# Performance work log

Measured on AMD Instinct MI355X. Metric: run time of the kernel, lower is better.

The kernel has to match this reference:

```python
import jax, jax.numpy as jnp
import numpy as np

N_NODES = 100000
N_EDGES = 1600000
D = 64
LN_EPS = 1e-5


def gcn_layer(x, src, dst, adv, W, b, g, be):
    # message: softmax(log(adv), dst) == adv / segment_sum(adv)[dst]  (per-target-node normalization)
    denom = jax.ops.segment_sum(adv, dst, num_segments=N_NODES)  # [N]
    att = adv / denom[dst]                                       # [E]
    msg = x[src] * att[:, None]                                  # [E, D] gather-multiply
    aggr = jax.ops.segment_sum(msg, dst, num_segments=N_NODES)   # [N, D] scatter-add
    # update: LayerNorm(Dropout(Linear(gelu(aggr) + x)))  (dropout = identity in eval)
    h = jax.nn.gelu(aggr, approximate=False) + x
    h = h @ W + b
    mu = jnp.mean(h, axis=-1, keepdims=True)
    var = jnp.mean((h - mu) ** 2, axis=-1, keepdims=True)
    return (h - mu) * jax.lax.rsqrt(var + LN_EPS) * g + be


def setup_inputs() -> dict:
    key = jax.random.key(0)
    ks = jax.random.split(key, 8)
    scale = 1.0 / np.sqrt(D)
    node_attr = jax.random.normal(ks[0], (N_NODES, D), jnp.float32)
    edge_index = jax.random.randint(ks[1], (2, N_EDGES), 0, N_NODES)
    batch_idx = jnp.zeros((N_NODES,), jnp.int32)
    adv_att0 = jax.random.uniform(ks[2], (N_EDGES,), jnp.float32) + 1e-3
    adv_att1 = jax.random.uniform(ks[3], (N_EDGES,), jnp.float32) + 1e-3
    W0 = jax.random.uniform(ks[4], (D, D), jnp.float32, -scale, scale)
    W1 = jax.random.uniform(ks[5], (D, D), jnp.float32, -scale, scale)
    b0 = jnp.zeros((D,), jnp.float32)
    b1 = jnp.zeros((D,), jnp.float32)
    g0 = jnp.ones((D,), jnp.float32)
    g1 = jnp.ones((D,), jnp.float32)
    be0 = jnp.zeros((D,), jnp.float32)
    be1 = jnp.zeros((D,), jnp.float32)
    return {"node_attr": node_attr, "edge_index": edge_index, "batch_idx": batch_idx,
            "adv_att0": adv_att0, "adv_att1": adv_att1,
            "W0": W0, "b0": b0, "g0": g0, "be0": be0,
            "W1": W1, "b1": b1, "g1": g1, "be1": be1}


def reference(node_attr, edge_index, batch_idx, adv_att0, adv_att1,
              W0, b0, g0, be0, W1, b1, g1, be1):
    src = edge_index[0]  # j (source)
    dst = edge_index[1]  # i (target)
    h = gcn_layer(node_attr, src, dst, adv_att0, W0, b0, g0, be0)
    h = gcn_layer(h, src, dst, adv_att1, W1, b1, g1, be1)
    return h  # node_level=True -> per-node representations [N, D]
```

## Files before the change

kernel.cpp:

```cpp
#include <hip/hip_runtime.h>
#include <math.h>

#define N_NODES 100000
#define N_EDGES 1600000
#define D 64
#define LN_EPS 1e-5f
#define NQ (N_EDGES / 4)
#define NODE_RANGE 12500
#define CAP 48

typedef int v2i __attribute__((ext_vector_type(2)));
typedef int v4i __attribute__((ext_vector_type(4)));

__device__ __forceinline__ unsigned short f2b(float f) {
    unsigned u = __float_as_uint(f);
    return (unsigned short)((u + 0x7FFFu + ((u >> 16) & 1u)) >> 16);
}
__device__ __forceinline__ unsigned pk2(float lo, float hi) {
    return (unsigned)f2b(lo) | ((unsigned)f2b(hi) << 16);
}
__device__ __forceinline__ float b2f(unsigned short u) {
    return __uint_as_float((unsigned)u << 16);
}

__global__ void k_tobf16z(const float4* __restrict__ in4, uint4* __restrict__ out4,
                          int* __restrict__ cnt) {
    int i = blockIdx.x * 256 + threadIdx.x;
    if (i < N_NODES) cnt[i] = 0;
    float4 a = in4[2 * i];
    float4 c = in4[2 * i + 1];
    uint4 o;
    o.x = pk2(a.x, a.y);
    o.y = pk2(a.z, a.w);
    o.z = pk2(c.x, c.y);
    o.w = pk2(c.z, c.w);
    out4[i] = o;
}

__global__ void k_bucket(const int* __restrict__ src, const v4i* __restrict__ dst4,
                         const float* __restrict__ adv0, const float* __restrict__ adv1,
                         int* __restrict__ cnt, v2i* __restrict__ rec) {
    const int g = blockIdx.x & 7;
    const int lb = blockIdx.x >> 3;
    const int nlb = gridDim.x >> 3;
    const int lo = g * NODE_RANGE, hi = lo + NODE_RANGE;
    for (int q = lb * 256 + threadIdx.x; q < NQ; q += nlb * 256) {
        v4i d = dst4[q];
        int e = q * 4;
#pragma unroll
        for (int c = 0; c < 4; ++c) {
            int dd = (c == 0) ? d.x : (c == 1) ? d.y : (c == 2) ? d.z : d.w;
            if (dd >= lo && dd < hi) {
                int p = atomicAdd(&cnt[dd], 1);
                if (p < CAP) {
                    int s = src[e + c];
                    float a0 = adv0[e + c];
                    float a1 = adv1[e + c];
                    v2i r;
                    r.x = s;
                    r.y = (int)pk2(a0, a1);
                    __builtin_nontemporal_store(r, &rec[(size_t)p * N_NODES + dd]);
                }
            }
        }
    }
}

template <int LAYER>
__global__ __launch_bounds__(256) void k_layer(const float* __restrict__ xres,
                                               const unsigned short* __restrict__ xb,
                                               const v2i* __restrict__ rec,
                                               const int* __restrict__ cnt,
                                               const float* __restrict__ W,
                                               const float* __restrict__ bb,
                                               const float* __restrict__ gg,
                                               const float* __restrict__ be,
                                               float* __restrict__ outf,
                                               unsigned short* __restrict__ outb) {
    const int lane = threadIdx.x & 63;
    const int wid = threadIdx.x >> 6;
    const int nodeA = blockIdx.x * 8 + wid;
    const int nodeB = nodeA + 4;
    const int nA = min(cnt[nodeA], CAP);
    const int nB = min(cnt[nodeB], CAP);

    const int slot = lane >> 3;
    const int fgrp = lane & 7;
    const int bpbase = slot << 2;

    float accA[8], accB[8];
#pragma unroll
    for (int i = 0; i < 8; ++i) { accA[i] = 0.f; accB[i] = 0.f; }

    int svA = 0, aviA = 0, svB = 0, aviB = 0;
    if (lane < nA) {
        v2i r = rec[(size_t)lane * N_NODES + nodeA];
        svA = r.x;
        unsigned pa = (unsigned)r.y;
        aviA = (int)(LAYER ? (pa & 0xFFFF0000u) : (pa << 16));
    }
    if (lane < nB) {
        v2i r = rec[(size_t)lane * N_NODES + nodeB];
        svB = r.x;
        unsigned pa = (unsigned)r.y;
        aviB = (int)(LAYER ? (pa & 0xFFFF0000u) : (pa << 16));
    }
    float sadvA = __int_as_float(aviA);
    float sadvB = __int_as_float(aviB);

    const int nmax = max(nA, nB);
    for (int j0 = 0; j0 < nmax; j0 += 8) {
        const int idx = (j0 << 2) + bpbase;
        if (j0 < nA) {
            int s = __builtin_amdgcn_ds_bpermute(idx, svA);
            float a = __int_as_float(__builtin_amdgcn_ds_bpermute(idx, aviA));
            uint4 u = *(const uint4*)(xb + (unsigned)s * D + (fgrp << 3));
            accA[0] = fmaf(__uint_as_float(u.x << 16), a, accA[0]);
            accA[1] = fmaf(__uint_as_float(u.x & 0xFFFF0000u), a, accA[1]);
            accA[2] = fmaf(__uint_as_float(u.y << 16), a, accA[2]);
            accA[3] = fmaf(__uint_as_float(u.y & 0xFFFF0000u), a, accA[3]);
            accA[4] = fmaf(__uint_as_float(u.z << 16), a, accA[4]);
            accA[5] = fmaf(__uint_as_float(u.z & 0xFFFF0000u), a, accA[5]);
            accA[6] = fmaf(__uint_as_float(u.w << 16), a, accA[6]);
            accA[7] = fmaf(__uint_as_float(u.w & 0xFFFF0000u), a, accA[7]);
        }
        if (j0 < nB) {
            int s = __builtin_amdgcn_ds_bpermute(idx, svB);
            float a = __int_as_float(__builtin_amdgcn_ds_bpermute(idx, aviB));
            uint4 u = *(const uint4*)(xb + (unsigned)s * D + (fgrp << 3));
            accB[0] = fmaf(__uint_as_float(u.x << 16), a, accB[0]);
            accB[1] = fmaf(__uint_as_float(u.x & 0xFFFF0000u), a, accB[1]);
            accB[2] = fmaf(__uint_as_float(u.y << 16), a, accB[2]);
            accB[3] = fmaf(__uint_as_float(u.y & 0xFFFF0000u), a, accB[3]);
            accB[4] = fmaf(__uint_as_float(u.z << 16), a, accB[4]);
            accB[5] = fmaf(__uint_as_float(u.z & 0xFFFF0000u), a, accB[5]);
            accB[6] = fmaf(__uint_as_float(u.w << 16), a, accB[6]);
            accB[7] = fmaf(__uint_as_float(u.w & 0xFFFF0000u), a, accB[7]);
        }
    }
#pragma unroll
    for (int m = 8; m <= 32; m <<= 1) {
#pragma unroll
        for (int i = 0; i < 8; ++i) {
            accA[i] += __shfl_xor(accA[i], m, 64);
            accB[i] += __shfl_xor(accB[i], m, 64);
        }
    }
    for (int m = 32; m; m >>= 1) {
        sadvA += __shfl_xor(sadvA, m, 64);
        sadvB += __shfl_xor(sadvB, m, 64);
    }

    __shared__ float hs[8][D];
    __shared__ float pp[4][8][D];
    if (slot == 0) {
#pragma unroll
        for (int i = 0; i < 8; ++i) {
            hs[wid][lane * 8 + i] = accA[i];
            hs[4 + wid][lane * 8 + i] = accB[i];
        }
    }
    float aggrA = (nA > 0) ? hs[wid][lane] / sadvA : 0.f;
    float aggrB = (nB > 0) ? hs[4 + wid][lane] / sadvB : 0.f;

    float xvA = (LAYER == 0) ? xres[(unsigned)(nodeA * D) + lane]
                             : b2f(xb[(unsigned)(nodeA * D) + lane]);
    float xvB = (LAYER == 0) ? xres[(unsigned)(nodeB * D) + lane]
                             : b2f(xb[(unsigned)(nodeB * D) + lane]);
    float geA = 0.5f * aggrA;
    float geB = 0.5f * aggrB;
    hs[wid][lane] = fmaf(geA, erff(aggrA * 0.70710678118654752f), geA + xvA);
    hs[4 + wid][lane] = fmaf(geB, erff(aggrB * 0.70710678118654752f), geB + xvB);
    __syncthreads();

    float py[8];
#pragma unroll
    for (int i = 0; i < 8; ++i) py[i] = 0.f;
    const float* wp = W + (wid * 16) * D + lane;
#pragma unroll
    for (int k4 = 0; k4 < 4; ++k4) {
        float w0 = wp[(k4 * 4 + 0) * D];
        float w1 = wp[(k4 * 4 + 1) * D];
        float w2 = wp[(k4 * 4 + 2) * D];
        float w3 = wp[(k4 * 4 + 3) * D];
#pragma unroll
        for (int nn = 0; nn < 8; ++nn) {
            float4 hv = *(const float4*)&hs[nn][wid * 16 + k4 * 4];
            py[nn] = fmaf(hv.x, w0, fmaf(hv.y, w1, fmaf(hv.z, w2, fmaf(hv.w, w3, py[nn]))));
        }
    }
#pragma unroll
    for (int nn = 0; nn < 8; ++nn) pp[wid][nn][lane] = py[nn];
    __syncthreads();

    const float bl = bb[lane], gl = gg[lane], bel = be[lane];
#pragma unroll
    for (int half = 0; half < 2; ++half) {
        const int row = wid + half * 4;
        const int node = blockIdx.x * 8 + row;
        float acc2 = bl + ((pp[0][row][lane] + pp[1][row][lane]) +
                           (pp[2][row][lane] + pp[3][row][lane]));
        float s = acc2;
        for (int m = 32; m; m >>= 1) s += __shfl_xor(s, m, 64);
        float mu = s * (1.f / 64.f);
        float dv = acc2 - mu;
        float v2 = dv * dv;
        for (int m = 32; m; m >>= 1) v2 += __shfl_xor(v2, m, 64);
        float var = v2 * (1.f / 64.f);
        float res = dv * rsqrtf(var + LN_EPS) * gl + bel;
        if (LAYER == 0)
            outb[(unsigned)(node * D) + lane] = f2b(res);
        else
            __builtin_nontemporal_store(res, outf + (unsigned)(node * D) + lane);
    }
}

extern "C" void kernel_launch(void* const* d_in, const int* in_sizes, int n_in,
                              void* d_out, int out_size, void* d_ws, size_t ws_size,
                              hipStream_t stream) {
    const float* node_attr = (const float*)d_in[0];
    const int* edge_index = (const int*)d_in[1];
    const float* adv0 = (const float*)d_in[3];
    const float* adv1 = (const float*)d_in[4];
    const float* W0 = (const float*)d_in[5];
    const float* b0 = (const float*)d_in[6];
    const float* g0 = (const float*)d_in[7];
    const float* be0 = (const float*)d_in[8];
    const float* W1 = (const float*)d_in[9];
    const float* b1 = (const float*)d_in[10];
    const float* g1 = (const float*)d_in[11];
    const float* be1 = (const float*)d_in[12];

    const int* src = edge_index;
    const v4i* dst4 = (const v4i*)(edge_index + N_EDGES);

    v2i* rec = (v2i*)d_ws;
    unsigned short* h1b = (unsigned short*)(rec + (size_t)N_NODES * CAP);
    int* cnt = (int*)(h1b + (size_t)N_NODES * D);

    float* out = (float*)d_out;
    unsigned short* xb0 = (unsigned short*)d_out;

    k_tobf16z<<<3125, 256, 0, stream>>>((const float4*)node_attr, (uint4*)xb0, cnt);

    k_bucket<<<4096, 256, 0, stream>>>(src, dst4, adv0, adv1, cnt, rec);

    k_layer<0><<<N_NODES / 8, 256, 0, stream>>>(node_attr, xb0, rec, cnt,
                                                W0, b0, g0, be0, nullptr, h1b);
    k_layer<1><<<N_NODES / 8, 256, 0, stream>>>(nullptr, h1b, rec, cnt,
                                                W1, b1, g1, be1, out, nullptr);
}
```

Measured before the change: 235.7 us.

## Make layer kernel persistent with register-resident weights and packed FMAs

Each layer kernel now runs a fixed grid of 2048 blocks that loop grid-stride over 8-node groups, instead of one block per group. Each thread loads its 16-row slice of W and the bias and LayerNorm parameters into registers once per block rather than once per group. The gather-accumulate loop now uses two-wide float vector FMAs, which may map to packed FP32 instructions. The aim is to cut block launch overhead and repeated weight loads. In exchange, register pressure rises and there may be fewer waves in flight to hide gather latency.

```diff
diff --git a/kernel.cpp b/kernel.cpp
--- a/kernel.cpp
+++ b/kernel.cpp
@@ -8,9 +8,11 @@
 #define NQ (N_EDGES / 4)
 #define NODE_RANGE 12500
 #define CAP 48
+#define NGRP (N_NODES / 8)
 
 typedef int v2i __attribute__((ext_vector_type(2)));
 typedef int v4i __attribute__((ext_vector_type(4)));
+typedef float v2f __attribute__((ext_vector_type(2)));
 
 __device__ __forceinline__ unsigned short f2b(float f) {
     unsigned u = __float_as_uint(f);
@@ -79,139 +81,154 @@
                                                unsigned short* __restrict__ outb) {
     const int lane = threadIdx.x & 63;
     const int wid = threadIdx.x >> 6;
-    const int nodeA = blockIdx.x * 8 + wid;
-    const int nodeB = nodeA + 4;
-    const int nA = min(cnt[nodeA], CAP);
-    const int nB = min(cnt[nodeB], CAP);
-
     const int slot = lane >> 3;
     const int fgrp = lane & 7;
     const int bpbase = slot << 2;
 
-    float accA[8], accB[8];
-#pragma unroll
-    for (int i = 0; i < 8; ++i) { accA[i] = 0.f; accB[i] = 0.f; }
-
-    int svA = 0, aviA = 0, svB = 0, aviB = 0;
-    if (lane < nA) {
-        v2i r = rec[(size_t)lane * N_NODES + nodeA];
-        svA = r.x;
-        unsigned pa = (unsigned)r.y;
-        aviA = (int)(LAYER ? (pa & 0xFFFF0000u) : (pa << 16));
+    float wreg[16];
+    {
+        const float* wp = W + (wid * 16) * D + lane;
+#pragma unroll
+        for (int k = 0; k < 16; ++k) wreg[k] = wp[k * D];
     }
-    if (lane < nB) {
-        v2i r = rec[(size_t)lane * N_NODES + nodeB];
-        svB = r.x;
-        unsigned pa = (unsigned)r.y;
-        aviB = (int)(LAYER ? (pa & 0xFFFF0000u) : (pa << 16));
-    }
-    float sadvA = __int_as_float(aviA);
-    float sadvB = __int_as_float(aviB);
-
-    const int nmax = max(nA, nB);
-    for (int j0 = 0; j0 < nmax; j0 += 8) {
-        const int idx = (j0 << 2) + bpbase;
-        if (j0 < nA) {
-            int s = __builtin_amdgcn_ds_bpermute(idx, svA);
-            float a = __int_as_float(__builtin_amdgcn_ds_bpermute(idx, aviA));
-            uint4 u = *(const uint4*)(xb + (unsigned)s * D + (fgrp << 3));
-            accA[0] = fmaf(__uint_as_float(u.x << 16), a, accA[0]);
-            accA[1] = fmaf(__uint_as_float(u.x & 0xFFFF0000u), a, accA[1]);
-            accA[2] = fmaf(__uint_as_float(u.y << 16), a, accA[2]);
-            accA[3] = fmaf(__uint_as_float(u.y & 0xFFFF0000u), a, accA[3]);
-            accA[4] = fmaf(__uint_as_float(u.z << 16), a, accA[4]);
-            accA[5] = fmaf(__uint_as_float(u.z & 0xFFFF0000u), a, accA[5]);
-            accA[6] = fmaf(__uint_as_float(u.w << 16), a, accA[6]);
-            accA[7] = fmaf(__uint_as_float(u.w & 0xFFFF0000u), a, accA[7]);
-        }
-        if (j0 < nB) {
-            int s = __builtin_amdgcn_ds_bpermute(idx, svB);
-            float a = __int_as_float(__builtin_amdgcn_ds_bpermute(idx, aviB));
-            uint4 u = *(const uint4*)(xb + (unsigned)s * D + (fgrp << 3));
-            accB[0] = fmaf(__uint_as_float(u.x << 16), a, accB[0]);
-            accB[1] = fmaf(__uint_as_float(u.x & 0xFFFF0000u), a, accB[1]);
-            accB[2] = fmaf(__uint_as_float(u.y << 16), a, accB[2]);
-            accB[3] = fmaf(__uint_as_float(u.y & 0xFFFF0000u), a, accB[3]);
-            accB[4] = fmaf(__uint_as_float(u.z << 16), a, accB[4]);
-            accB[5] = fmaf(__uint_as_float(u.z & 0xFFFF0000u), a, accB[5]);
-            accB[6] = fmaf(__uint_as_float(u.w << 16), a, accB[6]);
-            accB[7] = fmaf(__uint_as_float(u.w & 0xFFFF0000u), a, accB[7]);
-        }
-    }
-#pragma unroll
-    for (int m = 8; m <= 32; m <<= 1) {
-#pragma unroll
-        for (int i = 0; i < 8; ++i) {
-            accA[i] += __shfl_xor(accA[i], m, 64);
-            accB[i] += __shfl_xor(accB[i], m, 64);
-        }
-    }
-    for (int m = 32; m; m >>= 1) {
-        sadvA += __shfl_xor(sadvA, m, 64);
-        sadvB += __shfl_xor(sadvB, m, 64);
-    }
+    const float bl = bb[lane], gl = gg[lane], bel = be[lane];
 
     __shared__ float hs[8][D];
     __shared__ float pp[4][8][D];
-    if (slot == 0) {
-#pragma unroll
-        for (int i = 0; i < 8; ++i) {
-            hs[wid][lane * 8 + i] = accA[i];
-            hs[4 + wid][lane * 8 + i] = accB[i];
-        }
-    }
-    float aggrA = (nA > 0) ? hs[wid][lane] / sadvA : 0.f;
-    float aggrB = (nB > 0) ? hs[4 + wid][lane] / sadvB : 0.f;
-
-    float xvA = (LAYER == 0) ? xres[(unsigned)(nodeA * D) + lane]
-                             : b2f(xb[(unsigned)(nodeA * D) + lane]);
-    float xvB = (LAYER == 0) ? xres[(unsigned)(nodeB * D) + lane]
-                             : b2f(xb[(unsigned)(nodeB * D) + lane]);
-    float geA = 0.5f * aggrA;
-    float geB = 0.5f * aggrB;
-    hs[wid][lane] = fmaf(geA, erff(aggrA * 0.70710678118654752f), geA + xvA);
-    hs[4 + wid][lane] = fmaf(geB, erff(aggrB * 0.70710678118654752f), geB + xvB);
-    __syncthreads();
-
-    float py[8];
-#pragma unroll
-    for (int i = 0; i < 8; ++i) py[i] = 0.f;
-    const float* wp = W + (wid * 16) * D + lane;
-#pragma unroll
-    for (int k4 = 0; k4 < 4; ++k4) {
-        float w0 = wp[(k4 * 4 + 0) * D];
-        float w1 = wp[(k4 * 4 + 1) * D];
-        float w2 = wp[(k4 * 4 + 2) * D];
-        float w3 = wp[(k4 * 4 + 3) * D];
-#pragma unroll
-        for (int nn = 0; nn < 8; ++nn) {
-            float4 hv = *(const float4*)&hs[nn][wid * 16 + k4 * 4];
-            py[nn] = fmaf(hv.x, w0, fmaf(hv.y, w1, fmaf(hv.z, w2, fmaf(hv.w, w3, py[nn]))));
-        }
-    }
-#pragma unroll
-    for (int nn = 0; nn < 8; ++nn) pp[wid][nn][lane] = py[nn];
-    __syncthreads();
-
-    const float bl = bb[lane], gl = gg[lane], bel = be[lane];
-#pragma unroll
-    for (int half = 0; half < 2; ++half) {
-        const int row = wid + half * 4;
-        const int node = blockIdx.x * 8 + row;
-        float acc2 = bl + ((pp[0][row][lane] + pp[1][row][lane]) +
-                           (pp[2][row][lane] + pp[3][row][lane]));
-        float s = acc2;
-        for (int m = 32; m; m >>= 1) s += __shfl_xor(s, m, 64);
-        float mu = s * (1.f / 64.f);
-        float dv = acc2 - mu;
-        float v2 = dv * dv;
-        for (int m = 32; m; m >>= 1) v2 += __shfl_xor(v2, m, 64);
-        float var = v2 * (1.f / 64.f);
-        float res = dv * rsqrtf(var + LN_EPS) * gl + bel;
-        if (LAYER == 0)
-            outb[(unsigned)(node * D) + lane] = f2b(res);
-        else
-            __builtin_nontemporal_store(res, outf + (unsigned)(node * D) + lane);
+
+    for (int g = blockIdx.x; g < NGRP; g += gridDim.x) {
+        const int nodeA = g * 8 + wid;
+        const int nodeB = nodeA + 4;
+        const int nA = min(cnt[nodeA], CAP);
+        const int nB = min(cnt[nodeB], CAP);
+
+        v2f accA[4], accB[4];
+#pragma unroll
+        for (int i = 0; i < 4; ++i) { accA[i] = (v2f)0.f; accB[i] = (v2f)0.f; }
+
+        int svA = 0, aviA = 0, svB = 0, aviB = 0;
+        if (lane < nA) {
+            v2i r = rec[(size_t)lane * N_NODES + nodeA];
+            svA = r.x;
+            unsigned pa = (unsigned)r.y;
+            aviA = (int)(LAYER ? (pa & 0xFFFF0000u) : (pa << 16));
+        }
+        if (lane < nB) {
+            v2i r = rec[(size_t)lane * N_NODES + nodeB];
+            svB = r.x;
+            unsigned pa = (unsigned)r.y;
+            aviB = (int)(LAYER ? (pa & 0xFFFF0000u) : (pa << 16));
+        }
+        float sadvA = __int_as_float(aviA);
+        float sadvB = __int_as_float(aviB);
+
+        const int nmax = max(nA, nB);
+        for (int j0 = 0; j0 < nmax; j0 += 8) {
+            const int idx = (j0 << 2) + bpbase;
+            if (j0 < nA) {
+                int s = __builtin_amdgcn_ds_bpermute(idx, svA);
+                float a = __int_as_float(__builtin_amdgcn_ds_bpermute(idx, aviA));
+                v2f av = {a, a};
+                uint4 u = *(const uint4*)(xb + (unsigned)s * D + (fgrp << 3));
+                v2f x0 = {__uint_as_float(u.x << 16), __uint_as_float(u.x & 0xFFFF0000u)};
+                v2f x1 = {__uint_as_float(u.y << 16), __uint_as_float(u.y & 0xFFFF0000u)};
+                v2f x2 = {__uint_as_float(u.z << 16), __uint_as_float(u.z & 0xFFFF0000u)};
+                v2f x3 = {__uint_as_float(u.w << 16), __uint_as_float(u.w & 0xFFFF0000u)};
+                accA[0] = __builtin_elementwise_fma(x0, av, accA[0]);
+                accA[1] = __builtin_elementwise_fma(x1, av, accA[1]);
+                accA[2] = __builtin_elementwise_fma(x2, av, accA[2]);
+                accA[3] = __builtin_elementwise_fma(x3, av, accA[3]);
+            }
+            if (j0 < nB) {
+                int s = __builtin_amdgcn_ds_bpermute(idx, svB);
+                float a = __int_as_float(__builtin_amdgcn_ds_bpermute(idx, aviB));
+                v2f av = {a, a};
+                uint4 u = *(const uint4*)(xb + (unsigned)s * D + (fgrp << 3));
+                v2f x0 = {__uint_as_float(u.x << 16), __uint_as_float(u.x & 0xFFFF0000u)};
+                v2f x1 = {__uint_as_float(u.y << 16), __uint_as_float(u.y & 0xFFFF0000u)};
+                v2f x2 = {__uint_as_float(u.z << 16), __uint_as_float(u.z & 0xFFFF0000u)};
+                v2f x3 = {__uint_as_float(u.w << 16), __uint_as_float(u.w & 0xFFFF0000u)};
+                accB[0] = __builtin_elementwise_fma(x0, av, accB[0]);
+                accB[1] = __builtin_elementwise_fma(x1, av, accB[1]);
+                accB[2] = __builtin_elementwise_fma(x2, av, accB[2]);
+                accB[3] = __builtin_elementwise_fma(x3, av, accB[3]);
+            }
+        }
+#pragma unroll
+        for (int m = 8; m <= 32; m <<= 1) {
+#pragma unroll
+            for (int i = 0; i < 4; ++i) {
+                accA[i].x += __shfl_xor(accA[i].x, m, 64);
+                accA[i].y += __shfl_xor(accA[i].y, m, 64);
+                accB[i].x += __shfl_xor(accB[i].x, m, 64);
+                accB[i].y += __shfl_xor(accB[i].y, m, 64);
+            }
+        }
+        for (int m = 32; m; m >>= 1) {
+            sadvA += __shfl_xor(sadvA, m, 64);
+            sadvB += __shfl_xor(sadvB, m, 64);
+        }
+
+        if (slot == 0) {
+#pragma unroll
+            for (int i = 0; i < 4; ++i) {
+                hs[wid][lane * 8 + 2 * i] = accA[i].x;
+                hs[wid][lane * 8 + 2 * i + 1] = accA[i].y;
+                hs[4 + wid][lane * 8 + 2 * i] = accB[i].x;
+                hs[4 + wid][lane * 8 + 2 * i + 1] = accB[i].y;
+            }
+        }
+        float aggrA = (nA > 0) ? hs[wid][lane] / sadvA : 0.f;
+        float aggrB = (nB > 0) ? hs[4 + wid][lane] / sadvB : 0.f;
+
+        float xvA = (LAYER == 0) ? xres[(unsigned)(nodeA * D) + lane]
+                                 : b2f(xb[(unsigned)(nodeA * D) + lane]);
+        float xvB = (LAYER == 0) ? xres[(unsigned)(nodeB * D) + lane]
+                                 : b2f(xb[(unsigned)(nodeB * D) + lane]);
+        float geA = 0.5f * aggrA;
+        float geB = 0.5f * aggrB;
+        hs[wid][lane] = fmaf(geA, erff(aggrA * 0.70710678118654752f), geA + xvA);
+        hs[4 + wid][lane] = fmaf(geB, erff(aggrB * 0.70710678118654752f), geB + xvB);
+        __syncthreads();
+
+        float py[8];
+#pragma unroll
+        for (int i = 0; i < 8; ++i) py[i] = 0.f;
+#pragma unroll
+        for (int k4 = 0; k4 < 4; ++k4) {
+            float w0 = wreg[k4 * 4 + 0];
+            float w1 = wreg[k4 * 4 + 1];
+            float w2 = wreg[k4 * 4 + 2];
+            float w3 = wreg[k4 * 4 + 3];
+#pragma unroll
+            for (int nn = 0; nn < 8; ++nn) {
+                float4 hv = *(const float4*)&hs[nn][wid * 16 + k4 * 4];
+                py[nn] = fmaf(hv.x, w0, fmaf(hv.y, w1, fmaf(hv.z, w2, fmaf(hv.w, w3, py[nn]))));
+            }
+        }
+#pragma unroll
+        for (int nn = 0; nn < 8; ++nn) pp[wid][nn][lane] = py[nn];
+        __syncthreads();
+
+#pragma unroll
+        for (int half = 0; half < 2; ++half) {
+            const int row = wid + half * 4;
+            const int node = g * 8 + row;
+            float acc2 = bl + ((pp[0][row][lane] + pp[1][row][lane]) +
+                               (pp[2][row][lane] + pp[3][row][lane]));
+            float s = acc2;
+            for (int m = 32; m; m >>= 1) s += __shfl_xor(s, m, 64);
+            float mu = s * (1.f / 64.f);
+            float dv = acc2 - mu;
+            float v2 = dv * dv;
+            for (int m = 32; m; m >>= 1) v2 += __shfl_xor(v2, m, 64);
+            float var = v2 * (1.f / 64.f);
+            float res = dv * rsqrtf(var + LN_EPS) * gl + bel;
+            if (LAYER == 0)
+                outb[(unsigned)(node * D) + lane] = f2b(res);
+            else
+                __builtin_nontemporal_store(res, outf + (unsigned)(node * D) + lane);
+        }
     }
 }
 
@@ -245,8 +262,8 @@
 
     k_bucket<<<4096, 256, 0, stream>>>(src, dst4, adv0, adv1, cnt, rec);
 
-    k_layer<0><<<N_NODES / 8, 256, 0, stream>>>(node_attr, xb0, rec, cnt,
-                                                W0, b0, g0, be0, nullptr, h1b);
-    k_layer<1><<<N_NODES / 8, 256, 0, stream>>>(nullptr, h1b, rec, cnt,
-                                                W1, b1, g1, be1, out, nullptr);
-}
+    k_layer<0><<<2048, 256, 0, stream>>>(node_attr, xb0, rec, cnt,
+                                         W0, b0, g0, be0, nullptr, h1b);
+    k_layer<1><<<2048, 256, 0, stream>>>(nullptr, h1b, rec, cnt,
+                                         W1, b1, g1, be1, out, nullptr);
+}
```

Result: slower. 272.9 us (+15.8%).
